# Performance work log

Measured on AMD Instinct MI355X. Metric: run time of the kernel, lower is better.

The kernel has to match this reference:

```python
import jax, jax.numpy as jnp
import numpy as np

N = 100000   # nodes per layer
E = 600000   # edges per block
FIN = 256    # raw feature dim
H = 128      # hidden_size
C = 47       # n_classes
L = 3        # num_layers = n_layers + 1
NOUT = 10000 # seed nodes
GEN_EPS = 1e-7
T = 1.0
LN_EPS = 1e-5


def setup_inputs() -> dict:
    key = jax.random.key(0)
    ks = jax.random.split(key, 10)
    return {
        "x": jax.random.normal(ks[0], (N, FIN), jnp.float32),
        "src": jax.random.randint(ks[1], (L - 1, E), 0, N),
        "dst": jax.random.randint(ks[2], (L - 1, E), 0, N),
        "node_map": jax.random.randint(ks[3], (L - 1, N), 0, N),
        "final_map": jax.random.randint(ks[4], (NOUT,), 0, N),
        "enc_w": jax.random.normal(ks[5], (FIN, H), jnp.float32) * 0.05,
        "enc_b": jnp.zeros((H,), jnp.float32),
        "gcn_w": jax.random.normal(ks[6], (L, H, H), jnp.float32) * 0.05,
        "gcn_b": jnp.zeros((L, H), jnp.float32),
        "ln_g": jnp.ones((L, H), jnp.float32),
        "ln_b": jnp.zeros((L, H), jnp.float32),
        "pred_w": jax.random.normal(ks[7], (H, C), jnp.float32) * 0.05,
        "pred_b": jnp.zeros((C,), jnp.float32),
    }


def _layer_norm(h, g, b):
    mu = jnp.mean(h, axis=-1, keepdims=True)
    var = jnp.mean(jnp.square(h - mu), axis=-1, keepdims=True)
    return (h - mu) * jax.lax.rsqrt(var + LN_EPS) * g + b


def _gen_conv(h, src, dst, w, b):
    # GENConv, aggr='softmax', mlp_layers=1, no edge_attr, no msg_norm.
    m = jax.nn.relu(h[src]) + GEN_EPS                      # [E, H] messages
    # per-destination, per-feature segment softmax with temperature T
    mx = jax.ops.segment_max(m * T, dst, num_segments=N)   # [N, H]
    e = jnp.exp(m * T - mx[dst])                           # [E, H]
    denom = jax.ops.segment_sum(e, dst, num_segments=N)    # [N, H]
    alpha = e / (denom[dst] + 1e-16)
    agg = jax.ops.segment_sum(m * alpha, dst, num_segments=N)  # [N, H]
    return (agg + h) @ w + b                               # residual + Linear (MLP)


def reference(x, src, dst, node_map, final_map, enc_w, enc_b,
              gcn_w, gcn_b, ln_g, ln_b, pred_w, pred_b):
    h = x @ enc_w + enc_b                                  # node_features_encoder
    h = _gen_conv(h, src[0], dst[0], gcn_w[0], gcn_b[0])   # gcns[0] with block-0 edges
    for layer in range(1, L):                              # res+ block
        h2 = jax.nn.relu(_layer_norm(h, ln_g[layer - 1], ln_b[layer - 1]))
        # dropout is identity in eval mode (p applied with training=False)
        # gcns[layer] uses the edge_index set BEFORE this iteration's move
        h = _gen_conv(h2, src[layer - 1], dst[layer - 1],
                      gcn_w[layer], gcn_b[layer]) + h
        h = h[node_map[layer - 1]]                         # nf_move_layer_to gather
    h = jax.nn.relu(_layer_norm(h, ln_g[L - 1], ln_b[L - 1]))
    h = h @ pred_w + pred_b                                # node_pred_linear
    h = h[final_map]                                       # seed-node extraction
    return jax.nn.log_softmax(h, axis=-1)
```

## Files before the change

kernel.cpp:

```cpp
#include <hip/hip_runtime.h>
#include <hip/hip_bf16.h>
#include <hip/hip_fp16.h>

typedef unsigned short u16;
typedef unsigned int u32;

#define N_NODES 100000
#define N_EDGES 600000
#define FIN_D   256
#define HDIM    128
#define NCLS    47
#define NOUT_D  10000
#define NCHUNK  196
#define NP2     100352
#define PCH     4096
#define PNB     ((N_EDGES + PCH - 1) / PCH)

typedef short bf16x8 __attribute__((ext_vector_type(8)));
typedef float f32x4  __attribute__((ext_vector_type(4)));

#define GPTR(p) (const __attribute__((address_space(1))) u32*)(p)
#define LPTR(p) (__attribute__((address_space(3))) u32*)(p)

__device__ __forceinline__ float bf2f(u16 u) {
    union { u32 i; float f; } v; v.i = ((u32)u) << 16; return v.f;
}
__device__ __forceinline__ u16 f2bf(float f) {
    __hip_bfloat16 h = __float2bfloat16(f);
    return *reinterpret_cast<u16*>(&h);
}
__device__ __forceinline__ float loadF(const void* p, size_t i, bool f32) {
    if (f32) return ((const float*)p)[i];
    return bf2f(((const u16*)p)[i]);
}
__device__ __forceinline__ float wave_sum(float v) {
    #pragma unroll
    for (int o = 32; o > 0; o >>= 1) v += __shfl_xor(v, o, 64);
    return v;
}
__device__ __forceinline__ float wave_max(float v) {
    #pragma unroll
    for (int o = 32; o > 0; o >>= 1) v = fmaxf(v, __shfl_xor(v, o, 64));
    return v;
}
__device__ __forceinline__ int wave_sum_i(int v) {
    #pragma unroll
    for (int o = 32; o > 0; o >>= 1) v += __shfl_xor(v, o, 64);
    return v;
}
__device__ __forceinline__ int block_excl_scan_256(int v, int* wsum) {
    int lane = threadIdx.x & 63, wv = threadIdx.x >> 6;
    int inc = v;
    #pragma unroll
    for (int off = 1; off < 64; off <<= 1) {
        int u = __shfl_up(inc, off, 64);
        if (lane >= off) inc += u;
    }
    if (lane == 63) wsum[wv] = inc;
    __syncthreads();
    if (threadIdx.x == 0) {
        int a = 0;
        #pragma unroll
        for (int w = 0; w < 4; ++w) { int t = wsum[w]; wsum[w] = a; a += t; }
    }
    __syncthreads();
    return inc - v + wsum[wv];
}

__global__ __launch_bounds__(256) void dtype_detect_kernel(
    const u16* __restrict__ x, int* __restrict__ flag)
{
    int i = blockIdx.x * 256 + threadIdx.x;
    u32 e = (x[i] >> 7) & 0xFF;
    unsigned long long b = __ballot(e >= 200);
    if ((threadIdx.x & 63) == 0) {
        int c = __popcll(b);
        if (c) atomicAdd(&flag[1], c);
    }
}

__global__ __launch_bounds__(256) void hist2_kernel(
    const int* __restrict__ dst, int* __restrict__ deg2, int egrid)
{
    int half = (blockIdx.x >= egrid) ? 1 : 0;
    int e = (blockIdx.x - half * egrid) * 256 + threadIdx.x;
    if (e < N_EDGES) atomicAdd(&deg2[half * NP2 + dst[half * N_EDGES + e]], 1);
}

__global__ __launch_bounds__(256) void csum2_kernel(
    const int* __restrict__ deg2, int* __restrict__ csum)
{
    __shared__ int ws[4];
    int half = (blockIdx.x >= NCHUNK) ? 1 : 0;
    int b = blockIdx.x - half * NCHUNK;
    int i0 = half * NP2 + b * 512 + threadIdx.x;
    int v = 0;
    if (b * 512 + threadIdx.x < N_NODES) v += deg2[i0];
    if (b * 512 + threadIdx.x + 256 < N_NODES) v += deg2[i0 + 256];
    v = wave_sum_i(v);
    int lane = threadIdx.x & 63, wv = threadIdx.x >> 6;
    if (lane == 0) ws[wv] = v;
    __syncthreads();
    if (threadIdx.x == 0)
        csum[blockIdx.x] = ws[0] + ws[1] + ws[2] + ws[3];
}

__global__ __launch_bounds__(256) void coff2_kernel(
    const int* __restrict__ csum, int* __restrict__ coff,
    int* __restrict__ bcur)
{
    __shared__ int wsum[4];
    int t = threadIdx.x;
    for (int h = 0; h < 2; ++h) {
        int v = (t < NCHUNK) ? csum[h * NCHUNK + t] : 0;
        int excl = block_excl_scan_256(v, wsum);
        if (t < NCHUNK) {
            coff[h * NCHUNK + t] = excl;
            bcur[(h * NCHUNK + t) * 16] = excl;
        }
        __syncthreads();
    }
}

__global__ __launch_bounds__(256) void scan2_kernel(
    const int* __restrict__ deg2, const int* __restrict__ coff,
    int* __restrict__ rp0, int* __restrict__ rp1)
{
    __shared__ int wsum[4];
    int half = (blockIdx.x >= NCHUNK) ? 1 : 0;
    int b = blockIdx.x - half * NCHUNK;
    const int* deg = deg2 + half * NP2;
    int* rp = half ? rp1 : rp0;
    int t = threadIdx.x;
    int i0 = b * 512 + 2 * t;
    int d0 = (i0 < N_NODES) ? deg[i0] : 0;
    int d1 = (i0 + 1 < N_NODES) ? deg[i0 + 1] : 0;
    int excl = block_excl_scan_256(d0 + d1, wsum);
    int base = coff[half * NCHUNK + b] + excl;
    if (i0 < N_NODES)     rp[i0] = base;
    if (i0 + 1 < N_NODES) rp[i0 + 1] = base + d0;
    if (b == 0 && t == 0) rp[N_NODES] = N_EDGES;
}

__global__ __launch_bounds__(256) void bucket_part_kernel(
    const int* __restrict__ src, const int* __restrict__ dst,
    const int* __restrict__ comp1,
    int* __restrict__ bcur, int2* __restrict__ tmp)
{
    __shared__ int hist[NCHUNK];
    __shared__ int base[NCHUNK];
    int half = (blockIdx.x >= PNB) ? 1 : 0;
    int b = blockIdx.x - half * PNB;
    int e0 = b * PCH;
    for (int i = threadIdx.x; i < NCHUNK; i += 256) hist[i] = 0;
    __syncthreads();

    int2 loc[16];
    #pragma unroll
    for (int t = 0; t < 16; ++t) {
        int e = e0 + t * 256 + threadIdx.x;
        loc[t].y = -1;
        if (e < N_EDGES) {
            int ge = half * N_EDGES + e;
            int d = dst[ge];
            int s = src[ge];
            if (half) s = comp1[s];
            loc[t] = make_int2(s, d);
            atomicAdd(&hist[d >> 9], 1);
        }
    }
    __syncthreads();
    for (int i = threadIdx.x; i < NCHUNK; i += 256) {
        int h = hist[i];
        base[i] = (h > 0) ? atomicAdd(&bcur[(half * NCHUNK + i) * 16], h) : 0;
        hist[i] = 0;
    }
    __syncthreads();
    #pragma unroll
    for (int t = 0; t < 16; ++t) {
        if (loc[t].y >= 0) {
            int bk = loc[t].y >> 9;
            int pos = base[bk] + atomicAdd(&hist[bk], 1);
            tmp[(size_t)half * N_EDGES + pos] = loc[t];
        }
    }
}

__global__ __launch_bounds__(256) void bucket_sort_kernel(
    const int2* __restrict__ tmp,
    const int* __restrict__ rp0, const int* __restrict__ rp1,
    const int* __restrict__ coff, const int* __restrict__ csum,
    int* __restrict__ ei0, int* __restrict__ ei1)
{
    __shared__ int cur[512];
    int half = (blockIdx.x >= NCHUNK) ? 1 : 0;
    int b = blockIdx.x - half * NCHUNK;
    const int* rp = half ? rp1 : rp0;
    int* ei = half ? ei1 : ei0;
    int n0 = b * 512;
    #pragma unroll
    for (int i = threadIdx.x; i < 512; i += 256) {
        int n = n0 + i;
        cur[i] = (n < N_NODES) ? rp[n] : 0;
    }
    __syncthreads();
    int beg = coff[half * NCHUNK + b];
    int end = beg + csum[half * NCHUNK + b];
    for (int i = beg + threadIdx.x; i < end; i += 256) {
        int2 p = tmp[(size_t)half * N_EDGES + i];
        int pos = atomicAdd(&cur[p.y & 511], 1);
        ei[pos] = p.x;
    }
}

__global__ __launch_bounds__(256) void pack_b_kernel(
    const void* __restrict__ enc_w, const void* __restrict__ gcn_w,
    const int* __restrict__ dt, u16* __restrict__ Bp)
{
    const bool f32 = (dt[1] > 16);
    int o = blockIdx.x * 256 + threadIdx.x;
    if (o >= 32768 + 3 * 16384) return;
    const void* srcp; size_t soff; int m;
    if (o < 32768) { srcp = enc_w; soff = 0; m = o; }
    else {
        int l = (o - 32768) >> 14;
        srcp = gcn_w; soff = (size_t)l * 16384; m = (o - 32768) & 16383;
    }
    int j    = m & 7;
    int lane = (m >> 3) & 63;
    int ct   = (m >> 9) & 7;
    int kidx = m >> 12;
    int k = kidx * 32 + (lane >> 4) * 8 + j;
    int n = ct * 16 + (lane & 15);
    Bp[o] = f2bf(loadF(srcp, soff + (size_t)k * HDIM + n, f32));
}

__global__ __launch_bounds__(256, 2) void enc_gemm_kernel(
    const void* __restrict__ Araw, const u16* __restrict__ Bp,
    const void* __restrict__ bias, const int* __restrict__ dt,
    u16* __restrict__ OutBF)
{
    extern __shared__ char SH[];
    const bool f32 = (dt[1] > 16);
    const int tid  = threadIdx.x;
    const int w    = tid >> 6;
    const int lane = tid & 63;
    const int quad = lane >> 4;
    const int cl   = lane & 15;
    const int m0   = blockIdx.x * 16;

    #pragma unroll
    for (int i = 0; i < 16; ++i) {
        int off = (w * 16 + i) * 1024;
        __builtin_amdgcn_global_load_lds(
            GPTR((const char*)Bp + off + lane * 16),
            LPTR(SH + off), 16, 0, 0);
    }
    if (f32) {
        #pragma unroll
        for (int i = 0; i < 4; ++i) {
            int row = w * 4 + i;
            int src = (lane * 16) ^ ((row & 7) << 4);
            __builtin_amdgcn_global_load_lds(
                GPTR((const char*)Araw + (size_t)(m0 + row) * 1024 + src),
                LPTR(SH + 65536 + row * 1024), 16, 0, 0);
        }
    } else {
        #pragma unroll
        for (int i = 0; i < 2; ++i) {
            int r0 = (w * 2 + i) * 2;
            int row = r0 + (lane >> 5);
            int src = ((lane & 31) * 16) ^ ((row & 7) << 4);
            __builtin_amdgcn_global_load_lds(
                GPTR((const char*)Araw + (size_t)(m0 + row) * 512 + src),
                LPTR(SH + 65536 + r0 * 512), 16, 0, 0);
        }
    }

    f32x4 acc[2];
    acc[0] = (f32x4){0.f, 0.f, 0.f, 0.f};
    acc[1] = (f32x4){0.f, 0.f, 0.f, 0.f};
    const int ct0 = w * 2;
    const int swz = (cl & 7) << 4;

    __syncthreads();

    #pragma unroll
    for (int k = 0; k < 8; ++k) {
        bf16x8 av;
        if (f32) {
            const char* rb = SH + 65536 + cl * 1024;
            int lo = (k * 128 + quad * 32) ^ swz;
            float4 v0 = *(const float4*)(rb + lo);
            float4 v1 = *(const float4*)(rb + (lo ^ 16));
            union { u32 u[4]; bf16x8 v; } cv;
            cv.u[0] = (u32)f2bf(v0.x) | ((u32)f2bf(v0.y) << 16);
            cv.u[1] = (u32)f2bf(v0.z) | ((u32)f2bf(v0.w) << 16);
            cv.u[2] = (u32)f2bf(v1.x) | ((u32)f2bf(v1.y) << 16);
            cv.u[3] = (u32)f2bf(v1.z) | ((u32)f2bf(v1.w) << 16);
            av = cv.v;
        } else {
            const char* rb = SH + 65536 + cl * 512;
            av = *(const bf16x8*)(rb + ((k * 64 + quad * 16) ^ swz));
        }
        #pragma unroll
        for (int c = 0; c < 2; ++c) {
            bf16x8 b = *(const bf16x8*)(SH + k * 8192 + (ct0 + c) * 1024 + lane * 16);
            acc[c] = __builtin_amdgcn_mfma_f32_16x16x32_bf16(av, b, acc[c], 0, 0, 0);
        }
    }

    #pragma unroll
    for (int reg = 0; reg < 4; ++reg) {
        int grow = m0 + quad * 4 + reg;
        #pragma unroll
        for (int c = 0; c < 2; ++c) {
            int col = (ct0 + c) * 16 + cl;
            float v = acc[c][reg] + loadF(bias, col, f32);
            OutBF[(size_t)grow * HDIM + col] = f2bf(v);
        }
    }
}

template<bool OWN_MAP>
__global__ __launch_bounds__(256) void agg_msg_kernel(
    const int* __restrict__ rp, const int* __restrict__ eidx,
    const u16* __restrict__ HBin, const int* __restrict__ own_map,
    u16* __restrict__ Amsg)
{
    int wave = threadIdx.x >> 6;
    int lane = threadIdx.x & 63;
    int n = blockIdx.x * 4 + wave;
    if (n >= N_NODES) return;
    const u32* HB32 = (const u32*)HBin;
    int nn = OWN_MAP ? own_map[n] : n;
    u32 own = HB32[(size_t)nn * 64 + lane];
    int beg = rp[n], end = rp[n + 1];
    float den0 = 0.f, den1 = 0.f, num0 = 0.f, num1 = 0.f;
    for (int j0 = beg; j0 < end; j0 += 8) {
        int cnt = end - j0; if (cnt > 8) cnt = 8;
        int ss[8];
        #pragma unroll
        for (int t = 0; t < 8; ++t) {
            int j = j0 + t;
            ss[t] = eidx[j < end ? j : end - 1];
        }
        u32 hh[8];
        #pragma unroll
        for (int t = 0; t < 8; ++t)
            hh[t] = HB32[(size_t)ss[t] * 64 + lane];
        #pragma unroll
        for (int t = 0; t < 8; ++t) {
            float valid = (t < cnt) ? 1.f : 0.f;
            float m0 = fmaxf(bf2f((u16)(hh[t] & 0xffff)), 0.f) + 1e-7f;
            float m1 = fmaxf(bf2f((u16)(hh[t] >> 16)),    0.f) + 1e-7f;
            float e0 = __expf(m0) * valid, e1 = __expf(m1) * valid;
            den0 += e0; num0 += m0 * e0;
            den1 += e1; num1 += m1 * e1;
        }
    }
    float a0 = num0 / (den0 + 1e-16f) + bf2f((u16)(own & 0xffff));
    float a1 = num1 / (den1 + 1e-16f) + bf2f((u16)(own >> 16));
    ((u32*)Amsg)[(size_t)n * 64 + lane] = (u32)f2bf(a0) | ((u32)f2bf(a1) << 16);
}

template<bool RES, bool OWN_MAP, bool WRITE_LN>
__global__ __launch_bounds__(256) void conv_gemm_kernel(
    const u16* __restrict__ Amsg, const int* __restrict__ own_map,
    const u16* __restrict__ Bp, int Bpbase,
    const void* __restrict__ bias, int biasoff,
    const __half* __restrict__ Resid,
    const void* __restrict__ lng, const void* __restrict__ lnb, int lnoff,
    const int* __restrict__ dt,
    __half* __restrict__ OutH, u16* __restrict__ HBout)
{
    const bool f32 = (dt[1] > 16);
    __shared__ u16 Bsh[16384];
    const int tid  = threadIdx.x;
    const int w    = tid >> 6;
    const int lane = tid & 63;
    const int quad = lane >> 4;
    const int cl   = lane & 15;
    const int m0   = blockIdx.x * 64;

    {
        const uint4* bsrc = (const uint4*)(Bp + Bpbase);
        uint4* bdst = (uint4*)Bsh;
        #pragma unroll
        for (int j = 0; j < 8; ++j)
            bdst[j * 256 + tid] = bsrc[j * 256 + tid];
    }

    int arow = m0 + w * 16 + cl;
    if (arow >= N_NODES) arow = N_NODES - 1;
    bf16x8 afr[4];
    #pragma unroll
    for (int kidx = 0; kidx < 4; ++kidx)
        afr[kidx] = *(const bf16x8*)(Amsg + (size_t)arow * HDIM + kidx * 32 + quad * 8);

    __syncthreads();

    f32x4 acc[8];
    #pragma unroll
    for (int ct = 0; ct < 8; ++ct) acc[ct] = (f32x4){0.f, 0.f, 0.f, 0.f};
    #pragma unroll
    for (int kidx = 0; kidx < 4; ++kidx) {
        const u16* bb = Bsh + ((size_t)(kidx * 8) * 64 + lane) * 8;
        #pragma unroll
        for (int ct = 0; ct < 8; ++ct) {
            bf16x8 b = *(const bf16x8*)(bb + (size_t)ct * 512);
            acc[ct] = __builtin_amdgcn_mfma_f32_16x16x32_bf16(afr[kidx], b, acc[ct], 0, 0, 0);
        }
    }

    #pragma unroll
    for (int reg = 0; reg < 4; ++reg) {
        int n = m0 + w * 16 + quad * 4 + reg;
        if (n >= N_NODES) continue;
        size_t rrow = 0;
        if (RES) rrow = (size_t)(OWN_MAP ? own_map[n] : n) * HDIM;
        float v[8];
        float s1 = 0.f, s2 = 0.f;
        #pragma unroll
        for (int ct = 0; ct < 8; ++ct) {
            int col = ct * 16 + cl;
            float x = acc[ct][reg] + loadF(bias, biasoff + col, f32);
            if (RES) x += __half2float(Resid[rrow + col]);
            v[ct] = x;
            OutH[(size_t)n * HDIM + col] = __float2half(x);
            s1 += x; s2 += x * x;
        }
        if (WRITE_LN) {
            #pragma unroll
            for (int o = 1; o < 16; o <<= 1) {
                s1 += __shfl_xor(s1, o, 64);
                s2 += __shfl_xor(s2, o, 64);
            }
            float mu = s1 * (1.0f / 128.0f);
            float var = s2 * (1.0f / 128.0f) - mu * mu;
            float rs = rsqrtf(fmaxf(var, 0.f) + 1e-5f);
            #pragma unroll
            for (int ct = 0; ct < 8; ++ct) {
                int col = ct * 16 + cl;
                float y = fmaxf((v[ct] - mu) * rs * loadF(lng, lnoff + col, f32)
                                + loadF(lnb, lnoff + col, f32), 0.f);
                HBout[(size_t)n * HDIM + col] = f2bf(y);
            }
        }
    }
}

__global__ __launch_bounds__(64) void final_head_kernel(
    const __half* __restrict__ Hsrc, const int* __restrict__ map1,
    const int* __restrict__ fmap,
    const void* __restrict__ g, const void* __restrict__ b, int goff,
    const void* __restrict__ pw, const void* __restrict__ pb,
    const int* __restrict__ dt, void* __restrict__ out)
{
    const bool f32 = (dt[1] > 16);
    __shared__ float sh[HDIM];
    int i = blockIdx.x;
    int lane = threadIdx.x;
    int jj = map1[fmap[i]];
    __half2 hv = *((const __half2*)(Hsrc + (size_t)jj * HDIM) + lane);
    float2 v = __half22float2(hv);
    float mu = wave_sum(v.x + v.y) * (1.0f / 128.0f);
    float d0 = v.x - mu, d1 = v.y - mu;
    float var = wave_sum(d0 * d0 + d1 * d1) * (1.0f / 128.0f);
    float rs = rsqrtf(var + 1e-5f);
    int f0 = lane * 2;
    sh[f0]     = fmaxf(d0 * rs * loadF(g, goff + f0, f32)     + loadF(b, goff + f0, f32),     0.0f);
    sh[f0 + 1] = fmaxf(d1 * rs * loadF(g, goff + f0 + 1, f32) + loadF(b, goff + f0 + 1, f32), 0.0f);
    __syncthreads();
    float acc = -1e30f;
    if (lane < NCLS) {
        acc = loadF(pb, lane, f32);
        #pragma unroll 4
        for (int k = 0; k < HDIM; ++k)
            acc = fmaf(sh[k], loadF(pw, k * NCLS + lane, f32), acc);
    }
    float mx = wave_max(acc);
    float ex = (lane < NCLS) ? __expf(acc - mx) : 0.0f;
    float sum = wave_sum(ex);
    if (lane < NCLS) {
        float r = acc - mx - logf(sum);
        if (f32) ((float*)out)[(size_t)i * NCLS + lane] = r;
        else     ((u16*)out)[(size_t)i * NCLS + lane] = f2bf(r);
    }
}

extern "C" void kernel_launch(void* const* d_in, const int* in_sizes, int n_in,
                              void* d_out, int out_size, void* d_ws, size_t ws_size,
                              hipStream_t stream) {
    const void* x       = d_in[0];
    const int* src      = (const int*)d_in[1];
    const int* dst      = (const int*)d_in[2];
    const int* node_map = (const int*)d_in[3];
    const int* fmap     = (const int*)d_in[4];
    const void* enc_w   = d_in[5];
    const void* enc_b   = d_in[6];
    const void* gcn_w   = d_in[7];
    const void* gcn_b   = d_in[8];
    const void* ln_g    = d_in[9];
    const void* ln_b    = d_in[10];
    const void* pred_w  = d_in[11];
    const void* pred_b  = d_in[12];

    char* ws = (char*)d_ws;
    const size_t szH = (size_t)N_NODES * HDIM * sizeof(u16);
    __half* Pa  = (__half*)ws;  ws += szH;
    __half* Pb  = (__half*)ws;  ws += szH;
    u16*   HBa  = (u16*)ws;     ws += szH;
    u16*   HBb  = (u16*)ws;     ws += szH;
    u16*   Amsg = (u16*)ws;     ws += szH;
    int*   FLAG = (int*)ws;     ws += 1024;
    u16*   Bp   = (u16*)ws;     ws += (size_t)(32768 + 3 * 16384) * 2 + 1024;
    int*  deg2  = (int*)ws;  ws += (size_t)2 * NP2 * 4;
    int*  rp0   = (int*)ws;  ws += (size_t)(N_NODES + 2) * 4;
    int*  rp1   = (int*)ws;  ws += (size_t)(N_NODES + 2) * 4;
    int*  ei0   = (int*)ws;  ws += (size_t)N_EDGES * 4;
    int*  ei1   = (int*)ws;  ws += (size_t)N_EDGES * 4;
    int2* tmp   = (int2*)ws; ws += (size_t)2 * N_EDGES * 8;
    int*  csum  = (int*)ws;  ws += 2048;
    int*  coff  = (int*)ws;  ws += 2048;
    int*  bcur  = (int*)ws;  ws += (size_t)2 * NCHUNK * 16 * 4 + 1024;

    dim3 blk(256);
    const int ggrid = (N_NODES + 63) / 64;
    const int g16   = (N_NODES + 15) / 16;
    const int egrid = (N_EDGES + 255) / 256;
    const int agrid = (N_NODES + 3) / 4;
    const int pgrid = (32768 + 3 * 16384 + 255) / 256;

    hipMemsetAsync(FLAG, 0, 64, stream);
    dtype_detect_kernel<<<256, blk, 0, stream>>>((const u16*)x, FLAG);
    pack_b_kernel<<<pgrid, blk, 0, stream>>>(enc_w, gcn_w, FLAG, Bp);

    hipMemsetAsync(deg2, 0, (size_t)2 * NP2 * 4, stream);
    hist2_kernel<<<2 * egrid, blk, 0, stream>>>(dst, deg2, egrid);
    csum2_kernel<<<2 * NCHUNK, blk, 0, stream>>>(deg2, csum);
    coff2_kernel<<<1, blk, 0, stream>>>(csum, coff, bcur);
    scan2_kernel<<<2 * NCHUNK, blk, 0, stream>>>(deg2, coff, rp0, rp1);
    bucket_part_kernel<<<2 * PNB, blk, 0, stream>>>(src, dst, node_map, bcur, tmp);
    bucket_sort_kernel<<<2 * NCHUNK, blk, 0, stream>>>(tmp, rp0, rp1, coff, csum,
                                                       ei0, ei1);

    enc_gemm_kernel<<<g16, blk, 81920, stream>>>(x, Bp, enc_b, FLAG, HBa);

    agg_msg_kernel<false><<<agrid, blk, 0, stream>>>(rp0, ei0, HBa, nullptr, Amsg);
    conv_gemm_kernel<false, false, true><<<ggrid, blk, 0, stream>>>(
        Amsg, nullptr, Bp, 32768, gcn_b, 0, nullptr,
        ln_g, ln_b, 0, FLAG, Pa, HBb);

    agg_msg_kernel<false><<<agrid, blk, 0, stream>>>(rp0, ei0, HBb, nullptr, Amsg);
    conv_gemm_kernel<true, false, true><<<ggrid, blk, 0, stream>>>(
        Amsg, nullptr, Bp, 32768 + 16384, gcn_b, 128, Pa,
        ln_g, ln_b, 128, FLAG, Pb, HBa);

    agg_msg_kernel<true><<<agrid, blk, 0, stream>>>(rp1, ei1, HBa, node_map, Amsg);
    conv_gemm_kernel<true, true, false><<<ggrid, blk, 0, stream>>>(
        Amsg, node_map, Bp, 32768 + 2 * 16384, gcn_b, 256, Pb,
        ln_g, ln_b, 256, FLAG, Pa, nullptr);

    final_head_kernel<<<NOUT_D, dim3(64), 0, stream>>>(
        Pa, node_map + N_NODES, fmap, ln_g, ln_b, 256, pred_w, pred_b, FLAG,
        (void*)d_out);
}
```

Measured before the change: 575.3 us.

## Use direct global-to-LDS loads in aggregation and conv GEMM, halve partition chunk

The per-node softmax aggregation now fetches 16 neighbor feature rows per batch with global_load_lds into a per-wave shared buffer, using lane shuffles to distribute edge indices, instead of 8 per-lane register gathers. The conv GEMM loads both the weight tile and an XOR-swizzled A tile straight into LDS via global_load_lds rather than staging through registers. The bucket partition chunk size is halved to launch more blocks. The aims are more memory-level parallelism in the gather and less VGPR staging, at the cost of extra LDS use and explicit waitcnt barriers. The conv GEMM A-tile load also drops the previous clamp of out-of-range rows in the last block.

After: 571.2 us. No clear change (-0.7%).

```diff
diff --git a/kernel.cpp b/kernel.cpp
--- a/kernel.cpp
+++ b/kernel.cpp
@@ -13,7 +13,7 @@
 #define NOUT_D  10000
 #define NCHUNK  196
 #define NP2     100352
-#define PCH     4096
+#define PCH     2048
 #define PNB     ((N_EDGES + PCH - 1) / PCH)
 
 typedef short bf16x8 __attribute__((ext_vector_type(8)));
@@ -155,9 +155,9 @@
     for (int i = threadIdx.x; i < NCHUNK; i += 256) hist[i] = 0;
     __syncthreads();
 
-    int2 loc[16];
-    #pragma unroll
-    for (int t = 0; t < 16; ++t) {
+    int2 loc[8];
+    #pragma unroll
+    for (int t = 0; t < 8; ++t) {
         int e = e0 + t * 256 + threadIdx.x;
         loc[t].y = -1;
         if (e < N_EDGES) {
@@ -177,7 +177,7 @@
     }
     __syncthreads();
     #pragma unroll
-    for (int t = 0; t < 16; ++t) {
+    for (int t = 0; t < 8; ++t) {
         if (loc[t].y >= 0) {
             int bk = loc[t].y >> 9;
             int pos = base[bk] + atomicAdd(&hist[bk], 1);
@@ -328,6 +328,7 @@
     const u16* __restrict__ HBin, const int* __restrict__ own_map,
     u16* __restrict__ Amsg)
 {
+    __shared__ u32 RS[4][16][64];
     int wave = threadIdx.x >> 6;
     int lane = threadIdx.x & 63;
     int n = blockIdx.x * 4 + wave;
@@ -337,27 +338,34 @@
     u32 own = HB32[(size_t)nn * 64 + lane];
     int beg = rp[n], end = rp[n + 1];
     float den0 = 0.f, den1 = 0.f, num0 = 0.f, num1 = 0.f;
-    for (int j0 = beg; j0 < end; j0 += 8) {
-        int cnt = end - j0; if (cnt > 8) cnt = 8;
-        int ss[8];
-        #pragma unroll
-        for (int t = 0; t < 8; ++t) {
-            int j = j0 + t;
-            ss[t] = eidx[j < end ? j : end - 1];
-        }
-        u32 hh[8];
-        #pragma unroll
-        for (int t = 0; t < 8; ++t)
-            hh[t] = HB32[(size_t)ss[t] * 64 + lane];
-        #pragma unroll
-        for (int t = 0; t < 8; ++t) {
-            float valid = (t < cnt) ? 1.f : 0.f;
-            float m0 = fmaxf(bf2f((u16)(hh[t] & 0xffff)), 0.f) + 1e-7f;
-            float m1 = fmaxf(bf2f((u16)(hh[t] >> 16)),    0.f) + 1e-7f;
-            float e0 = __expf(m0) * valid, e1 = __expf(m1) * valid;
+    for (int c = beg; c < end; c += 16) {
+        int cnt = end - c; if (cnt > 16) cnt = 16;
+        int e = c + (lane & 15); if (e > end - 1) e = end - 1;
+        int ei = eidx[e];
+        int nI = (cnt + 3) >> 2;
+        #pragma unroll
+        for (int i = 0; i < 4; ++i) {
+            if (i < nI) {
+                int s = __shfl(ei, i * 4 + (lane >> 4), 64);
+                __builtin_amdgcn_global_load_lds(
+                    GPTR((const char*)HBin + (size_t)s * 256 + (lane & 15) * 16),
+                    LPTR(&RS[wave][i * 4][0]), 16, 0, 0);
+            }
+        }
+        asm volatile("s_waitcnt vmcnt(0)" ::: "memory");
+        __builtin_amdgcn_sched_barrier(0);
+        #pragma unroll
+        for (int t = 0; t < 16; ++t) {
+            if (t >= cnt) break;
+            u32 h = RS[wave][t][lane];
+            float m0 = fmaxf(bf2f((u16)(h & 0xffff)), 0.f) + 1e-7f;
+            float m1 = fmaxf(bf2f((u16)(h >> 16)),    0.f) + 1e-7f;
+            float e0 = __expf(m0), e1 = __expf(m1);
             den0 += e0; num0 += m0 * e0;
             den1 += e1; num1 += m1 * e1;
         }
+        asm volatile("s_waitcnt lgkmcnt(0)" ::: "memory");
+        __builtin_amdgcn_sched_barrier(0);
     }
     float a0 = num0 / (den0 + 1e-16f) + bf2f((u16)(own & 0xffff));
     float a1 = num1 / (den1 + 1e-16f) + bf2f((u16)(own >> 16));
@@ -376,6 +384,7 @@
 {
     const bool f32 = (dt[1] > 16);
     __shared__ u16 Bsh[16384];
+    __shared__ u16 Ash[8192];
     const int tid  = threadIdx.x;
     const int w    = tid >> 6;
     const int lane = tid & 63;
@@ -384,21 +393,32 @@
     const int m0   = blockIdx.x * 64;
 
     {
-        const uint4* bsrc = (const uint4*)(Bp + Bpbase);
-        uint4* bdst = (uint4*)Bsh;
-        #pragma unroll
-        for (int j = 0; j < 8; ++j)
-            bdst[j * 256 + tid] = bsrc[j * 256 + tid];
-    }
-
-    int arow = m0 + w * 16 + cl;
-    if (arow >= N_NODES) arow = N_NODES - 1;
+        const char* Bp2 = (const char*)(Bp + Bpbase);
+        #pragma unroll
+        for (int i = 0; i < 8; ++i)
+            __builtin_amdgcn_global_load_lds(
+                GPTR(Bp2 + i * 4096 + w * 1024 + lane * 16),
+                LPTR((char*)Bsh + i * 4096 + w * 1024), 16, 0, 0);
+        const char* Ab = (const char*)Amsg + (size_t)m0 * 256;
+        #pragma unroll
+        for (int i = 0; i < 4; ++i) {
+            int row_local = i * 16 + w * 4 + (lane >> 4);
+            int off = ((lane & 15) * 16) ^ ((row_local & 7) << 4);
+            __builtin_amdgcn_global_load_lds(
+                GPTR(Ab + (size_t)row_local * 256 + off),
+                LPTR((char*)Ash + i * 4096 + w * 1024), 16, 0, 0);
+        }
+    }
+
+    __syncthreads();
+
+    const int row_local = w * 16 + cl;
+    const char* ar = (const char*)Ash + row_local * 256;
+    const int akey = (row_local & 7) << 4;
     bf16x8 afr[4];
     #pragma unroll
     for (int kidx = 0; kidx < 4; ++kidx)
-        afr[kidx] = *(const bf16x8*)(Amsg + (size_t)arow * HDIM + kidx * 32 + quad * 8);
-
-    __syncthreads();
+        afr[kidx] = *(const bf16x8*)(ar + ((kidx * 64 + quad * 16) ^ akey));
 
     f32x4 acc[8];
     #pragma unroll
```
